# Kernel tuning notes

Hardware: AMD Instinct MI355X
Metric: run time of the kernel (lower is better)

The kernel has to match this reference:

```python
import jax, jax.numpy as jnp
import numpy as np

E = 8          # moe_expert_count
CAPACITY = 1024  # per-expert capacity C = S / E (capacity factor 1)


def _top1_gate(features, wg):
    """Top-1 gate with capacity, returning combine_weights [S,E,C],
    dispatch_mask [S,E,C], and load-balancing aux loss (standard Switch/BASE-style gate
    matching the (l_aux, combine_weights, dispatch_mask) interface used by BaseLayer)."""
    S, M = features.shape
    logits = features @ wg                      # [S, E]
    gates = jax.nn.softmax(logits, axis=-1)     # [S, E]
    idx = jnp.argmax(gates, axis=-1)            # [S] expert assignment
    mask1 = jax.nn.one_hot(idx, E, dtype=features.dtype)  # [S, E]
    # position of each token inside its expert's buffer (0-based, order of arrival)
    locations = jnp.cumsum(mask1, axis=0) - mask1          # [S, E]
    loc = jnp.sum(locations * mask1, axis=1).astype(jnp.int32)  # [S]
    keep = (loc < CAPACITY).astype(features.dtype)          # drop overflow tokens
    mask1 = mask1 * keep[:, None]
    gate_s = jnp.sum(gates * mask1, axis=1)                 # [S] gate prob of kept tokens
    loc_oh = jax.nn.one_hot(loc, CAPACITY, dtype=features.dtype)  # [S, C]
    combine = gate_s[:, None, None] * mask1[:, :, None] * loc_oh[:, None, :]  # [S,E,C]
    dispatch = (combine > 0).astype(features.dtype)
    # load-balance aux loss: E * sum(mean_prob_e * frac_tokens_e)
    me = jnp.mean(gates, axis=0)
    ce = jnp.mean(mask1, axis=0)
    l_aux = jnp.sum(me * ce) * E
    return l_aux, combine, dispatch


def setup_inputs() -> dict:
    key = jax.random.key(0)
    k0, k1, k2, k3 = jax.random.split(key, 4)
    B, T, M, H = 4, 2048, 512, 1024
    return {
        "hidden_states": jax.random.normal(k0, (B, T, M), dtype=jnp.float32),
        "wg": jax.random.normal(k1, (M, E), dtype=jnp.float32) * 0.02,
        "w1": jax.random.normal(k2, (E, M, H), dtype=jnp.float32) * 0.02,
        "b1": jnp.zeros((E, H), dtype=jnp.float32),
        "w2": jax.random.normal(k3, (E, H, M), dtype=jnp.float32) * 0.02,
        "b2": jnp.zeros((E, M), dtype=jnp.float32),
    }


def reference(hidden_states, wg, w1, b1, w2, b2):
    B, T, M = hidden_states.shape
    feats = hidden_states.reshape(-1, M)            # [S, M]
    l_aux, combine, dispatch = _top1_gate(feats, wg)
    # dense one-hot dispatch matmul: (E*C, S) @ (S, M) -> [E, C, M]
    dispatched = jnp.einsum('sec,sm->ecm', dispatch, feats)
    # per-expert FFN (BaseSublayer: Linear -> ReLU -> Linear)
    h = jax.nn.relu(jnp.einsum('ecm,emh->ech', dispatched, w1) + b1[:, None, :])
    expert_out = jnp.einsum('ech,ehn->ecn', h, w2) + b2[:, None, :]  # [E, C, M]
    # dense combine matmul: (S, E*C) @ (E*C, M) -> [S, M]
    combined = jnp.einsum('sec,ecn->sn', combine, expert_out)
    return combined.reshape(B, T, -1), l_aux
```

## Files before the change

kernel.cpp:

```cpp
#include <hip/hip_runtime.h>

#define S_TOK 8192
#define M_DIM 512
#define E_NUM 8
#define CAP   1024
#define H_DIM 1024
#define NGATE_BLK (S_TOK / 4)

typedef __attribute__((ext_vector_type(8))) short bf16x8;
typedef __attribute__((ext_vector_type(4))) float f32x4;

__device__ static inline unsigned short f2bf(float f) {
    unsigned int u = __float_as_uint(f);
    unsigned int r = (u + 0x7fffu + ((u >> 16) & 1u)) >> 16;
    return (unsigned short)r;
}

__device__ static inline void async_copy16(const void* g, void* l) {
    __builtin_amdgcn_global_load_lds(
        (const __attribute__((address_space(1))) void*)g,
        (__attribute__((address_space(3))) void*)l, 16, 0, 0);
}

__global__ __launch_bounds__(256) void prep_kernel(
    const float* __restrict__ feats, const float* __restrict__ wg,
    int* __restrict__ idx, float* __restrict__ gate_top,
    float* __restrict__ gates_psum, unsigned short* __restrict__ xb,
    const float* __restrict__ w1, unsigned short* __restrict__ w1t,
    const float* __restrict__ w2, unsigned short* __restrict__ w2t)
{
    __shared__ float gsh[4][8];
    __shared__ float tile[32][33];

    if (blockIdx.x < NGATE_BLK) {
        const int wave = threadIdx.x >> 6;
        const int lane = threadIdx.x & 63;
        const int s = blockIdx.x * 4 + wave;

        const float* xrow = feats + (size_t)s * M_DIM;
        const int m0 = lane * 8;

        const float4 va = *(const float4*)(xrow + m0);
        const float4 vb = *(const float4*)(xrow + m0 + 4);
        float xv[8] = {va.x, va.y, va.z, va.w, vb.x, vb.y, vb.z, vb.w};

        {
            bf16x8 o;
#pragma unroll
            for (int j = 0; j < 8; ++j) o[j] = (short)f2bf(xv[j]);
            *(bf16x8*)(xb + (size_t)s * M_DIM + m0) = o;
            if (blockIdx.x == 0 && wave == 0) {
                bf16x8 z = (bf16x8){0,0,0,0,0,0,0,0};
                *(bf16x8*)(xb + (size_t)S_TOK * M_DIM + m0) = z;
            }
        }

        float p[8];
#pragma unroll
        for (int e = 0; e < 8; ++e) p[e] = 0.f;
#pragma unroll
        for (int j = 0; j < 8; ++j) {
            const float4 wa = *(const float4*)(wg + (m0 + j) * 8);
            const float4 wb2 = *(const float4*)(wg + (m0 + j) * 8 + 4);
            const float x = xv[j];
            p[0] += x * wa.x;  p[1] += x * wa.y;  p[2] += x * wa.z;  p[3] += x * wa.w;
            p[4] += x * wb2.x; p[5] += x * wb2.y; p[6] += x * wb2.z; p[7] += x * wb2.w;
        }
#pragma unroll
        for (int e = 0; e < 8; ++e) {
            float v = p[e];
#pragma unroll
            for (int off = 1; off < 64; off <<= 1) v += __shfl_xor(v, off, 64);
            p[e] = v;
        }
        if (lane == 0) {
            float mx = p[0];
#pragma unroll
            for (int e = 1; e < 8; ++e) mx = fmaxf(mx, p[e]);
            float ex[8], sum = 0.f;
#pragma unroll
            for (int e = 0; e < 8; ++e) { ex[e] = expf(p[e] - mx); sum += ex[e]; }
            const float inv = 1.0f / sum;
            int best = 0; float bl = p[0];
#pragma unroll
            for (int e = 1; e < 8; ++e) { if (p[e] > bl) { bl = p[e]; best = e; } }
#pragma unroll
            for (int e = 0; e < 8; ++e) gsh[wave][e] = ex[e] * inv;
            idx[s] = best;
            gate_top[s] = ex[best] * inv;
        }
        __syncthreads();
        if (threadIdx.x < 8) {
            const int e = threadIdx.x;
            gates_psum[blockIdx.x * 8 + e] =
                gsh[0][e] + gsh[1][e] + gsh[2][e] + gsh[3][e];
        }
    } else {
        int b = blockIdx.x - NGATE_BLK;
        const float* src; unsigned short* dst;
        int e, k0, n0, K, N;
        if (b < 4096) {
            e = b >> 9; k0 = ((b >> 5) & 15) * 32; n0 = (b & 31) * 32;
            K = 512; N = 1024; src = w1; dst = w1t;
        } else {
            b -= 4096;
            e = b >> 9; k0 = ((b >> 4) & 31) * 32; n0 = (b & 15) * 32;
            K = 1024; N = 512; src = w2; dst = w2t;
        }
        const int t = threadIdx.x;
        const int r = t >> 3, c4 = (t & 7) * 4;
        {
            const float4 v = *(const float4*)(src + ((size_t)e * K + k0 + r) * N + n0 + c4);
            tile[r][c4 + 0] = v.x; tile[r][c4 + 1] = v.y;
            tile[r][c4 + 2] = v.z; tile[r][c4 + 3] = v.w;
        }
        __syncthreads();
        {
            ushort4 o;
            o.x = f2bf(tile[c4 + 0][r]); o.y = f2bf(tile[c4 + 1][r]);
            o.z = f2bf(tile[c4 + 2][r]); o.w = f2bf(tile[c4 + 3][r]);
            *(ushort4*)(dst + ((size_t)e * N + n0 + r) * K + k0 + c4) = o;
        }
    }
}

__global__ __launch_bounds__(256) void scan_kernel(
    const int* __restrict__ idx, const float* __restrict__ gate_top,
    const float* __restrict__ gates_psum,
    float* __restrict__ gate_final, int* __restrict__ token_list,
    int* __restrict__ kept, float* __restrict__ out)
{
    __shared__ int   cnts[256][9];
    __shared__ float wpart[4][8];
    __shared__ int   totals[8];
    __shared__ int   sdrop[7168];
    __shared__ int   dropctr;

    const int t = threadIdx.x;
    const int wv = t >> 6, ln = t & 63;
    const int base = t * 32;

    for (int i = t; i < E_NUM * CAP; i += 256) token_list[i] = S_TOK;
    if (t == 0) dropctr = 0;

    int c[8];
#pragma unroll
    for (int e = 0; e < 8; ++e) c[e] = 0;
    for (int i = 0; i < 32; ++i) {
        const int ei = idx[base + i];
#pragma unroll
        for (int e = 0; e < 8; ++e) c[e] += (ei == e) ? 1 : 0;
    }
    float g[8];
#pragma unroll
    for (int e = 0; e < 8; ++e) g[e] = 0.f;
    for (int i = 0; i < NGATE_BLK / 256; ++i) {
        const float* gp = gates_psum + (size_t)(t + 256 * i) * 8;
        const float4 a = *(const float4*)gp;
        const float4 b = *(const float4*)(gp + 4);
        g[0] += a.x; g[1] += a.y; g[2] += a.z; g[3] += a.w;
        g[4] += b.x; g[5] += b.y; g[6] += b.z; g[7] += b.w;
    }
#pragma unroll
    for (int e = 0; e < 8; ++e) cnts[t][e] = c[e];
#pragma unroll
    for (int e = 0; e < 8; ++e) {
        float v = g[e];
#pragma unroll
        for (int off = 1; off < 64; off <<= 1) v += __shfl_xor(v, off, 64);
        if (ln == 0) wpart[wv][e] = v;
    }
    __syncthreads();

#pragma unroll
    for (int ee = 0; ee < 2; ++ee) {
        const int e = wv * 2 + ee;
        int off = 0;
#pragma unroll
        for (int seg = 0; seg < 4; ++seg) {
            const int r = seg * 64 + ln;
            const int v = cnts[r][e];
            int incl = v;
#pragma unroll
            for (int d = 1; d < 64; d <<= 1) {
                const int nn = __shfl_up(incl, d, 64);
                if (ln >= d) incl += nn;
            }
            cnts[r][e] = incl - v + off;
            off += __shfl(incl, 63, 64);
        }
        if (ln == 0) {
            totals[e] = off;
            kept[e] = off < CAP ? off : CAP;
        }
    }
    __syncthreads();

    if (t == 0) {
        float l = 0.f;
        for (int e = 0; e < 8; ++e) {
            const float ms = wpart[0][e] + wpart[1][e] + wpart[2][e] + wpart[3][e];
            const int ke = totals[e] < CAP ? totals[e] : CAP;
            l += (ms / (float)S_TOK) * ((float)ke / (float)S_TOK);
        }
        out[(size_t)S_TOK * M_DIM] = l * (float)E_NUM;
    }

    int rc[8];
#pragma unroll
    for (int e = 0; e < 8; ++e) rc[e] = cnts[t][e];

    for (int i = 0; i < 32; ++i) {
        const int s = base + i;
        const int ei = idx[s];
        int loc = 0;
#pragma unroll
        for (int e = 0; e < 8; ++e) {
            if (ei == e) { loc = rc[e]; rc[e] = rc[e] + 1; }
        }
        const bool keepit = loc < CAP;
        gate_final[s] = keepit ? gate_top[s] : 0.f;
        if (keepit) {
            token_list[ei * CAP + loc] = s;
        } else {
            const int d = atomicAdd(&dropctr, 1);
            sdrop[d] = s;
        }
    }
    __syncthreads();

    const int nd = dropctr;
    for (int d = 0; d < nd; ++d) {
        const int s = sdrop[d];
        *(float2*)(out + (size_t)s * M_DIM + t * 2) = make_float2(0.f, 0.f);
    }
}

__global__ __launch_bounds__(256, 4) void ffn1_mfma(
    const unsigned short* __restrict__ xb, const unsigned short* __restrict__ w1t,
    const float* __restrict__ b1, const int* __restrict__ tok,
    const int* __restrict__ kept, unsigned short* __restrict__ h)
{
    const int b = blockIdx.x;
    const int e = b & 7;
    const int r = b >> 3;
    const int ct = r >> 4, nt = r & 15;
    const int c0 = ct * 128, n0 = nt * 64;
    if (c0 >= kept[e]) return;

    __shared__ __align__(16) short Alds[128 * 64];
    __shared__ __align__(16) short Blds[64 * 64];
    __shared__ int srow[128];

    const int t = threadIdx.x;
    const int wave = t >> 6, lane = t & 63;
    const int wm = wave & 1, wn = wave >> 1;
    const int q = lane >> 4, lr = lane & 15;

    if (t < 128) srow[t] = tok[e * CAP + c0 + t];
    __syncthreads();

    f32x4 acc[4][2];
#pragma unroll
    for (int mi = 0; mi < 4; ++mi)
#pragma unroll
        for (int ni = 0; ni < 2; ++ni) acc[mi][ni] = (f32x4){0.f, 0.f, 0.f, 0.f};

    for (int kb = 0; kb < M_DIM; kb += 64) {
        __syncthreads();
#pragma unroll
        for (int i = 0; i < 4; ++i) {
            const int lin = (i * 4 + wave) * 64 + lane;
            const int row = lin >> 3;
            const int ch = (lin & 7) ^ (row & 7);
            async_copy16(xb + (size_t)srow[row] * M_DIM + kb + ch * 8,
                         &Alds[lin * 8]);
        }
#pragma unroll
        for (int i = 0; i < 2; ++i) {
            const int lin = (i * 4 + wave) * 64 + lane;
            const int row = lin >> 3;
            const int ch = (lin & 7) ^ (row & 7);
            async_copy16(w1t + ((size_t)e * H_DIM + n0 + row) * M_DIM + kb + ch * 8,
                         &Blds[lin * 8]);
        }
        __syncthreads();

#pragma unroll
        for (int kk = 0; kk < 64; kk += 32) {
            const int cb = kk >> 3;
            bf16x8 af[4], bfv[2];
#pragma unroll
            for (int mi = 0; mi < 4; ++mi) {
                const int R = wm * 64 + mi * 16 + lr;
                af[mi] = *(const bf16x8*)(&Alds[(R * 8 + ((cb + q) ^ (R & 7))) * 8]);
            }
#pragma unroll
            for (int ni = 0; ni < 2; ++ni) {
                const int R = wn * 32 + ni * 16 + lr;
                bfv[ni] = *(const bf16x8*)(&Blds[(R * 8 + ((cb + q) ^ (R & 7))) * 8]);
            }
#pragma unroll
            for (int mi = 0; mi < 4; ++mi)
#pragma unroll
                for (int ni = 0; ni < 2; ++ni)
                    acc[mi][ni] = __builtin_amdgcn_mfma_f32_16x16x32_bf16(
                        af[mi], bfv[ni], acc[mi][ni], 0, 0, 0);
        }
    }

#pragma unroll
    for (int ni = 0; ni < 2; ++ni) {
        const int col = n0 + wn * 32 + ni * 16 + lr;
        const float bias = b1[e * H_DIM + col];
#pragma unroll
        for (int mi = 0; mi < 4; ++mi) {
            const int rowl = wm * 64 + mi * 16 + q * 4;
            const size_t basep = (size_t)(e * CAP + c0 + rowl) * H_DIM + col;
#pragma unroll
            for (int r2 = 0; r2 < 4; ++r2) {
                const float v = fmaxf(acc[mi][ni][r2] + bias, 0.f);
                h[basep + (size_t)r2 * H_DIM] = f2bf(v);
            }
        }
    }
}

__global__ __launch_bounds__(256, 4) void ffn2_mfma(
    const unsigned short* __restrict__ h, const unsigned short* __restrict__ w2t,
    const float* __restrict__ b2, const int* __restrict__ tok,
    const int* __restrict__ kept, const float* __restrict__ gate_final,
    float* __restrict__ out)
{
    const int b = blockIdx.x;
    const int e = b & 7;
    const int r = b >> 3;
    const int ct = r >> 3, nt = r & 7;
    const int c0 = ct * 64, n0 = nt * 64;
    if (c0 >= kept[e]) return;

    __shared__ __align__(16) short Alds[64 * 64];
    __shared__ __align__(16) short Blds[64 * 64];
    __shared__ int   stok[64];
    __shared__ float sgf[64];

    const int t = threadIdx.x;
    const int wave = t >> 6, lane = t & 63;
    const int wm = wave & 1, wn = wave >> 1;
    const int q = lane >> 4, lr = lane & 15;

    if (t < 64) {
        const int tk = tok[e * CAP + c0 + t];
        stok[t] = tk;
        sgf[t] = (tk != S_TOK) ? gate_final[tk] : 0.f;
    }

    f32x4 acc[2][2];
#pragma unroll
    for (int mi = 0; mi < 2; ++mi)
#pragma unroll
        for (int ni = 0; ni < 2; ++ni) acc[mi][ni] = (f32x4){0.f, 0.f, 0.f, 0.f};

    for (int kb = 0; kb < H_DIM; kb += 64) {
        __syncthreads();
#pragma unroll
        for (int i = 0; i < 2; ++i) {
            const int lin = (i * 4 + wave) * 64 + lane;
            const int row = lin >> 3;
            const int ch = (lin & 7) ^ (row & 7);
            async_copy16(h + (size_t)(e * CAP + c0 + row) * H_DIM + kb + ch * 8,
                         &Alds[lin * 8]);
        }
#pragma unroll
        for (int i = 0; i < 2; ++i) {
            const int lin = (i * 4 + wave) * 64 + lane;
            const int row = lin >> 3;
            const int ch = (lin & 7) ^ (row & 7);
            async_copy16(w2t + ((size_t)e * M_DIM + n0 + row) * H_DIM + kb + ch * 8,
                         &Blds[lin * 8]);
        }
        __syncthreads();

#pragma unroll
        for (int kk = 0; kk < 64; kk += 32) {
            const int cb = kk >> 3;
            bf16x8 af[2], bfv[2];
#pragma unroll
            for (int mi = 0; mi < 2; ++mi) {
                const int R = wm * 32 + mi * 16 + lr;
                af[mi] = *(const bf16x8*)(&Alds[(R * 8 + ((cb + q) ^ (R & 7))) * 8]);
            }
#pragma unroll
            for (int ni = 0; ni < 2; ++ni) {
                const int R = wn * 32 + ni * 16 + lr;
                bfv[ni] = *(const bf16x8*)(&Blds[(R * 8 + ((cb + q) ^ (R & 7))) * 8]);
            }
#pragma unroll
            for (int mi = 0; mi < 2; ++mi)
#pragma unroll
                for (int ni = 0; ni < 2; ++ni)
                    acc[mi][ni] = __builtin_amdgcn_mfma_f32_16x16x32_bf16(
                        af[mi], bfv[ni], acc[mi][ni], 0, 0, 0);
        }
    }

#pragma unroll
    for (int ni = 0; ni < 2; ++ni) {
        const int col = n0 + wn * 32 + ni * 16 + lr;
        const float bias = b2[e * M_DIM + col];
#pragma unroll
        for (int mi = 0; mi < 2; ++mi) {
            const int rowl = wm * 32 + mi * 16 + q * 4;
#pragma unroll
            for (int r2 = 0; r2 < 4; ++r2) {
                const int slot = rowl + r2;
                const int tokid = stok[slot];
                if (tokid != S_TOK) {
                    out[(size_t)tokid * M_DIM + col] = sgf[slot] * (acc[mi][ni][r2] + bias);
                }
            }
        }
    }
}

extern "C" void kernel_launch(void* const* d_in, const int* in_sizes, int n_in,
                              void* d_out, int out_size, void* d_ws, size_t ws_size,
                              hipStream_t stream) {
    const float* feats = (const float*)d_in[0];
    const float* wg    = (const float*)d_in[1];
    const float* w1    = (const float*)d_in[2];
    const float* b1    = (const float*)d_in[3];
    const float* w2    = (const float*)d_in[4];
    const float* b2    = (const float*)d_in[5];
    float* out = (float*)d_out;

    char* ws = (char*)d_ws;
    size_t off = 0;
    unsigned short* h   = (unsigned short*)(ws + off); off += (size_t)E_NUM * CAP * H_DIM * 2;
    unsigned short* xb  = (unsigned short*)(ws + off); off += (size_t)(S_TOK + 1) * M_DIM * 2;
    unsigned short* w1t = (unsigned short*)(ws + off); off += (size_t)E_NUM * H_DIM * M_DIM * 2;
    unsigned short* w2t = (unsigned short*)(ws + off); off += (size_t)E_NUM * M_DIM * H_DIM * 2;
    int*   idx        = (int*)(ws + off);   off += (size_t)S_TOK * 4;
    float* gate_top   = (float*)(ws + off); off += (size_t)S_TOK * 4;
    float* gate_final = (float*)(ws + off); off += (size_t)S_TOK * 4;
    float* gates_psum = (float*)(ws + off); off += (size_t)NGATE_BLK * 8 * 4;
    int*   token_list = (int*)(ws + off);   off += (size_t)S_TOK * 4;
    int*   kept       = (int*)(ws + off);   off += 64;
    (void)ws_size; (void)n_in; (void)in_sizes;

    prep_kernel<<<NGATE_BLK + 8192, 256, 0, stream>>>(
        feats, wg, idx, gate_top, gates_psum, xb, w1, w1t, w2, w2t);
    scan_kernel<<<1, 256, 0, stream>>>(idx, gate_top, gates_psum, gate_final,
                                       token_list, kept, out);
    ffn1_mfma<<<1024, 256, 0, stream>>>(xb, w1t, b1, token_list, kept, h);
    ffn2_mfma<<<1024, 256, 0, stream>>>(h, w2t, b2, token_list, kept,
                                        gate_final, out);
}
```

Before: 179.5 us.

## Double-buffer FFN GEMM LDS stages, enlarge weight transpose tiles, parallelize drop zeroing

Both expert FFN MFMA kernels now keep two LDS buffers, so the async global-to-LDS load of the next K-slice is issued while the current slice is computed. This overlaps memory latency with MFMA work. ffn1 occupancy drops to 3 blocks per CU because of the larger LDS footprint. The weight transpose/bf16 conversion in the prep kernel moves from 32x32 to 64x64 tiles with a quarter as many blocks, and the scan kernel zeroes dropped-token rows with all four waves and float4 stores instead of one row at a time.

```diff
diff --git a/kernel.cpp b/kernel.cpp
--- a/kernel.cpp
+++ b/kernel.cpp
@@ -30,7 +30,7 @@
     const float* __restrict__ w2, unsigned short* __restrict__ w2t)
 {
     __shared__ float gsh[4][8];
-    __shared__ float tile[32][33];
+    __shared__ float tile[64][65];
 
     if (blockIdx.x < NGATE_BLK) {
         const int wave = threadIdx.x >> 6;
@@ -99,27 +99,33 @@
         int b = blockIdx.x - NGATE_BLK;
         const float* src; unsigned short* dst;
         int e, k0, n0, K, N;
-        if (b < 4096) {
-            e = b >> 9; k0 = ((b >> 5) & 15) * 32; n0 = (b & 31) * 32;
+        if (b < 1024) {
+            e = b >> 7; const int rem = b & 127;
+            k0 = (rem >> 4) * 64; n0 = (rem & 15) * 64;
             K = 512; N = 1024; src = w1; dst = w1t;
         } else {
-            b -= 4096;
-            e = b >> 9; k0 = ((b >> 4) & 31) * 32; n0 = (b & 15) * 32;
+            b -= 1024;
+            e = b >> 7; const int rem = b & 127;
+            k0 = (rem >> 3) * 64; n0 = (rem & 7) * 64;
             K = 1024; N = 512; src = w2; dst = w2t;
         }
         const int t = threadIdx.x;
-        const int r = t >> 3, c4 = (t & 7) * 4;
-        {
-            const float4 v = *(const float4*)(src + ((size_t)e * K + k0 + r) * N + n0 + c4);
-            tile[r][c4 + 0] = v.x; tile[r][c4 + 1] = v.y;
-            tile[r][c4 + 2] = v.z; tile[r][c4 + 3] = v.w;
+        const int r = t >> 4, c4 = (t & 15) * 4;
+#pragma unroll
+        for (int i = 0; i < 4; ++i) {
+            const int row = r + i * 16;
+            const float4 v = *(const float4*)(src + ((size_t)e * K + k0 + row) * N + n0 + c4);
+            tile[row][c4 + 0] = v.x; tile[row][c4 + 1] = v.y;
+            tile[row][c4 + 2] = v.z; tile[row][c4 + 3] = v.w;
         }
         __syncthreads();
-        {
+#pragma unroll
+        for (int i = 0; i < 4; ++i) {
+            const int row = r + i * 16;
             ushort4 o;
-            o.x = f2bf(tile[c4 + 0][r]); o.y = f2bf(tile[c4 + 1][r]);
-            o.z = f2bf(tile[c4 + 2][r]); o.w = f2bf(tile[c4 + 3][r]);
-            *(ushort4*)(dst + ((size_t)e * N + n0 + r) * K + k0 + c4) = o;
+            o.x = f2bf(tile[c4 + 0][row]); o.y = f2bf(tile[c4 + 1][row]);
+            o.z = f2bf(tile[c4 + 2][row]); o.w = f2bf(tile[c4 + 3][row]);
+            *(ushort4*)(dst + ((size_t)e * N + n0 + row) * K + k0 + c4) = o;
         }
     }
 }
@@ -230,13 +236,15 @@
     __syncthreads();
 
     const int nd = dropctr;
-    for (int d = 0; d < nd; ++d) {
+    for (int d = wv; d < nd; d += 4) {
         const int s = sdrop[d];
-        *(float2*)(out + (size_t)s * M_DIM + t * 2) = make_float2(0.f, 0.f);
-    }
-}
-
-__global__ __launch_bounds__(256, 4) void ffn1_mfma(
+        float4 z = make_float4(0.f, 0.f, 0.f, 0.f);
+        *(float4*)(out + (size_t)s * M_DIM + ln * 4) = z;
+        *(float4*)(out + (size_t)s * M_DIM + 256 + ln * 4) = z;
+    }
+}
+
+__global__ __launch_bounds__(256, 3) void ffn1_mfma(
     const unsigned short* __restrict__ xb, const unsigned short* __restrict__ w1t,
     const float* __restrict__ b1, const int* __restrict__ tok,
     const int* __restrict__ kept, unsigned short* __restrict__ h)
@@ -248,8 +256,8 @@
     const int c0 = ct * 128, n0 = nt * 64;
     if (c0 >= kept[e]) return;
 
-    __shared__ __align__(16) short Alds[128 * 64];
-    __shared__ __align__(16) short Blds[64 * 64];
+    __shared__ __align__(16) short Alds[2][128 * 64];
+    __shared__ __align__(16) short Blds[2][64 * 64];
     __shared__ int srow[128];
 
     const int t = threadIdx.x;
@@ -260,21 +268,14 @@
     if (t < 128) srow[t] = tok[e * CAP + c0 + t];
     __syncthreads();
 
-    f32x4 acc[4][2];
-#pragma unroll
-    for (int mi = 0; mi < 4; ++mi)
-#pragma unroll
-        for (int ni = 0; ni < 2; ++ni) acc[mi][ni] = (f32x4){0.f, 0.f, 0.f, 0.f};
-
-    for (int kb = 0; kb < M_DIM; kb += 64) {
-        __syncthreads();
+    auto stage = [&](int buf, int kb) {
 #pragma unroll
         for (int i = 0; i < 4; ++i) {
             const int lin = (i * 4 + wave) * 64 + lane;
             const int row = lin >> 3;
             const int ch = (lin & 7) ^ (row & 7);
             async_copy16(xb + (size_t)srow[row] * M_DIM + kb + ch * 8,
-                         &Alds[lin * 8]);
+                         &Alds[buf][lin * 8]);
         }
 #pragma unroll
         for (int i = 0; i < 2; ++i) {
@@ -282,9 +283,22 @@
             const int row = lin >> 3;
             const int ch = (lin & 7) ^ (row & 7);
             async_copy16(w1t + ((size_t)e * H_DIM + n0 + row) * M_DIM + kb + ch * 8,
-                         &Blds[lin * 8]);
-        }
+                         &Blds[buf][lin * 8]);
+        }
+    };
+
+    f32x4 acc[4][2];
+#pragma unroll
+    for (int mi = 0; mi < 4; ++mi)
+#pragma unroll
+        for (int ni = 0; ni < 2; ++ni) acc[mi][ni] = (f32x4){0.f, 0.f, 0.f, 0.f};
+
+    stage(0, 0);
+
+    int cur = 0;
+    for (int kb = 0; kb < M_DIM; kb += 64) {
         __syncthreads();
+        if (kb + 64 < M_DIM) stage(cur ^ 1, kb + 64);
 
 #pragma unroll
         for (int kk = 0; kk < 64; kk += 32) {
@@ -293,12 +307,12 @@
 #pragma unroll
             for (int mi = 0; mi < 4; ++mi) {
                 const int R = wm * 64 + mi * 16 + lr;
-                af[mi] = *(const bf16x8*)(&Alds[(R * 8 + ((cb + q) ^ (R & 7))) * 8]);
+                af[mi] = *(const bf16x8*)(&Alds[cur][(R * 8 + ((cb + q) ^ (R & 7))) * 8]);
             }
 #pragma unroll
             for (int ni = 0; ni < 2; ++ni) {
                 const int R = wn * 32 + ni * 16 + lr;
-                bfv[ni] = *(const bf16x8*)(&Blds[(R * 8 + ((cb + q) ^ (R & 7))) * 8]);
+                bfv[ni] = *(const bf16x8*)(&Blds[cur][(R * 8 + ((cb + q) ^ (R & 7))) * 8]);
             }
 #pragma unroll
             for (int mi = 0; mi < 4; ++mi)
@@ -307,6 +321,7 @@
                     acc[mi][ni] = __builtin_amdgcn_mfma_f32_16x16x32_bf16(
                         af[mi], bfv[ni], acc[mi][ni], 0, 0, 0);
         }
+        cur ^= 1;
     }
 
 #pragma unroll
@@ -339,8 +354,8 @@
     const int c0 = ct * 64, n0 = nt * 64;
     if (c0 >= kept[e]) return;
 
-    __shared__ __align__(16) short Alds[64 * 64];
-    __shared__ __align__(16) short Blds[64 * 64];
+    __shared__ __align__(16) short Alds[2][64 * 64];
+    __shared__ __align__(16) short Blds[2][64 * 64];
     __shared__ int   stok[64];
     __shared__ float sgf[64];
 
@@ -355,21 +370,14 @@
         sgf[t] = (tk != S_TOK) ? gate_final[tk] : 0.f;
     }
 
-    f32x4 acc[2][2];
-#pragma unroll
-    for (int mi = 0; mi < 2; ++mi)
-#pragma unroll
-        for (int ni = 0; ni < 2; ++ni) acc[mi][ni] = (f32x4){0.f, 0.f, 0.f, 0.f};
-
-    for (int kb = 0; kb < H_DIM; kb += 64) {
-        __syncthreads();
+    auto stage = [&](int buf, int kb) {
 #pragma unroll
         for (int i = 0; i < 2; ++i) {
             const int lin = (i * 4 + wave) * 64 + lane;
             const int row = lin >> 3;
             const int ch = (lin & 7) ^ (row & 7);
             async_copy16(h + (size_t)(e * CAP + c0 + row) * H_DIM + kb + ch * 8,
-                         &Alds[lin * 8]);
+                         &Alds[buf][lin * 8]);
         }
 #pragma unroll
         for (int i = 0; i < 2; ++i) {
@@ -377,9 +385,22 @@
             const int row = lin >> 3;
             const int ch = (lin & 7) ^ (row & 7);
             async_copy16(w2t + ((size_t)e * M_DIM + n0 + row) * H_DIM + kb + ch * 8,
-                         &Blds[lin * 8]);
-        }
+                         &Blds[buf][lin * 8]);
+        }
+    };
+
+    f32x4 acc[2][2];
+#pragma unroll
+    for (int mi = 0; mi < 2; ++mi)
+#pragma unroll
+        for (int ni = 0; ni < 2; ++ni) acc[mi][ni] = (f32x4){0.f, 0.f, 0.f, 0.f};
+
+    stage(0, 0);
+
+    int cur = 0;
+    for (int kb = 0; kb < H_DIM; kb += 64) {
         __syncthreads();
+        if (kb + 64 < H_DIM) stage(cur ^ 1, kb + 64);
 
 #pragma unroll
         for (int kk = 0; kk < 64; kk += 32) {
@@ -388,12 +409,12 @@
 #pragma unroll
             for (int mi = 0; mi < 2; ++mi) {
                 const int R = wm * 32 + mi * 16 + lr;
-                af[mi] = *(const bf16x8*)(&Alds[(R * 8 + ((cb + q) ^ (R & 7))) * 8]);
+                af[mi] = *(const bf16x8*)(&Alds[cur][(R * 8 + ((cb + q) ^ (R & 7))) * 8]);
             }
 #pragma unroll
             for (int ni = 0; ni < 2; ++ni) {
                 const int R = wn * 32 + ni * 16 + lr;
-                bfv[ni] = *(const bf16x8*)(&Blds[(R * 8 + ((cb + q) ^ (R & 7))) * 8]);
+                bfv[ni] = *(const bf16x8*)(&Blds[cur][(R * 8 + ((cb + q) ^ (R & 7))) * 8]);
             }
 #pragma unroll
             for (int mi = 0; mi < 2; ++mi)
@@ -402,6 +423,7 @@
                     acc[mi][ni] = __builtin_amdgcn_mfma_f32_16x16x32_bf16(
                         af[mi], bfv[ni], acc[mi][ni], 0, 0, 0);
         }
+        cur ^= 1;
     }
 
 #pragma unroll
@@ -448,7 +470,7 @@
     int*   kept       = (int*)(ws + off);   off += 64;
     (void)ws_size; (void)n_in; (void)in_sizes;
 
-    prep_kernel<<<NGATE_BLK + 8192, 256, 0, stream>>>(
+    prep_kernel<<<NGATE_BLK + 2048, 256, 0, stream>>>(
         feats, wg, idx, gate_top, gates_psum, xb, w1, w1t, w2, w2t);
     scan_kernel<<<1, 256, 0, stream>>>(idx, gate_top, gates_psum, gate_final,
                                        token_list, kept, out);
```

Result: no change. 182.9 us (+1.9%).
